# Optimization experiments

Hardware: AMD Instinct MI355X
Metric: run time of the kernel (lower is better)

## Reference

```python
import jax, jax.numpy as jnp
import numpy as np

B, T, N, H, D = 8, 128, 170, 4, 16
F = H * D  # 64
LN_EPS = 1e-5
MASK_FILL = -(2.0 ** 15) + 1.0  # -32767, matches torch code


def setup_inputs() -> dict:
    key = jax.random.key(0)
    ks = jax.random.split(key, 16)
    s = 0.05
    def w(k):
        return jax.random.normal(k, (F, F), jnp.float32) * s
    def b(k):
        return jax.random.normal(k, (F,), jnp.float32) * s
    return {
        "x": jax.random.normal(ks[0], (B, T, N, F), jnp.float32),
        "te": jax.random.normal(ks[1], (B, T, N, F), jnp.float32),
        "Wq": w(ks[2]), "bq": b(ks[3]),
        "Wk": w(ks[4]), "bk": b(ks[5]),
        "Wv": w(ks[6]), "bv": b(ks[7]),
        "Wo": w(ks[8]), "bo": b(ks[9]),
        "Wf1": w(ks[10]), "bf1": b(ks[11]),
        "Wf2": w(ks[12]), "bf2": b(ks[13]),
    }


def _ln(v):
    # LayerNorm over last dim, elementwise_affine=False
    m = jnp.mean(v, axis=-1, keepdims=True)
    var = jnp.mean((v - m) ** 2, axis=-1, keepdims=True)
    return (v - m) / jnp.sqrt(var + LN_EPS)


def reference(x, te, Wq, bq, Wk, bk, Wv, bv, Wo, bo, Wf1, bf1, Wf2, bf2):
    x = x + te  # [B,T,N,F]
    # q/k/v projections (FeedForward with L=1 -> plain linear, no ReLU)
    q = (x @ Wq + bq).reshape(B, T, N, H, D)
    k = (x @ Wk + bk).reshape(B, T, N, H, D)
    v = (x @ Wv + bv).reshape(B, T, N, H, D)
    # attention over time axis, independent per node n and head h
    att = jnp.einsum('btnhd,bsnhd->bhnts', q, k) / jnp.sqrt(jnp.float32(D))
    causal = jnp.tril(jnp.ones((T, T), dtype=bool))  # keep s <= t
    att = jnp.where(causal[None, None, None, :, :], att, MASK_FILL)
    att = jax.nn.softmax(att, axis=-1)
    out = jnp.einsum('bhnts,bsnhd->btnhd', att, v).reshape(B, T, N, F)
    out = out @ Wo + bo  # ofc
    val = _ln(out + x)
    # ff: Linear-ReLU-Linear with residual + LN (res_ln=True)
    ff = jax.nn.relu(val @ Wf1 + bf1) @ Wf2 + bf2
    return _ln(ff + val)
```

## Files before the change

### kernel.cpp

```cpp
#include <hip/hip_runtime.h>

typedef __attribute__((ext_vector_type(8))) short short8;
typedef __attribute__((ext_vector_type(4))) float f32x4;
typedef __attribute__((ext_vector_type(16))) float f32x16;

#define B_ 8
#define T_ 128
#define N_ 170
#define F_ 64
#define ROWSTRIDE (N_ * F_)

union U4 { unsigned u[4]; short8 s; };

__device__ __forceinline__ unsigned short f2bf(float f) {
    union { float f; unsigned u; } v; v.f = f;
    unsigned r = v.u + 0x7fffu + ((v.u >> 16) & 1u);
    return (unsigned short)(r >> 16);
}
__device__ __forceinline__ unsigned cvtpk(float lo, float hi) {
    unsigned d;
    asm("v_cvt_pk_bf16_f32 %0, %1, %2" : "=v"(d) : "v"(lo), "v"(hi));
    return d;
}
__device__ __forceinline__ int swz128(int row, int byteInRow) {
    return row * 128 + (byteInRow ^ ((row & 7) << 4));
}
__device__ __forceinline__ int swz256(int row, int byteInRow) {
    return row * 256 + (byteInRow ^ ((row & 15) << 4));
}
__device__ __forceinline__ short8 ldfrag16(const char* base, int row0, int kbyte, int lane) {
    int row = row0 + (lane & 15);
    return *(const short8*)(base + swz128(row, kbyte + ((lane >> 4) << 4)));
}
__device__ __forceinline__ short8 ldfrag16w(const char* base, int row0, int kbyte, int lane) {
    int row = row0 + (lane & 15);
    return *(const short8*)(base + swz256(row, kbyte + ((lane >> 4) << 4)));
}
__device__ __forceinline__ short8 ldfrag32(const char* base, int row0, int colbyte, int lane) {
    int row = row0 + (lane & 31);
    return *(const short8*)(base + swz128(row, colbyte + ((lane >> 5) << 4)));
}
__device__ __forceinline__ short8 wfragT(const unsigned short* __restrict__ wT, int nt, int kc, int lane) {
    int j  = nt * 16 + (lane & 15);
    int k0 = kc * 32 + ((lane >> 4) & 3) * 8;
    return *(const short8*)(wT + j * 64 + k0);
}
__device__ __forceinline__ f32x4 zero4() {
    f32x4 v = {0.f, 0.f, 0.f, 0.f};
    return v;
}
__device__ __forceinline__ f32x16 zero16() {
    f32x16 v = {0.f, 0.f, 0.f, 0.f, 0.f, 0.f, 0.f, 0.f,
                0.f, 0.f, 0.f, 0.f, 0.f, 0.f, 0.f, 0.f};
    return v;
}
__device__ __forceinline__ float rmax16(const f32x16& v) {
    float a0 = fmaxf(v[0], v[1]),  a1 = fmaxf(v[2], v[3]);
    float a2 = fmaxf(v[4], v[5]),  a3 = fmaxf(v[6], v[7]);
    float a4 = fmaxf(v[8], v[9]),  a5 = fmaxf(v[10], v[11]);
    float a6 = fmaxf(v[12], v[13]), a7 = fmaxf(v[14], v[15]);
    float b0 = fmaxf(a0, a1), b1 = fmaxf(a2, a3);
    float b2 = fmaxf(a4, a5), b3 = fmaxf(a6, a7);
    return fmaxf(fmaxf(b0, b1), fmaxf(b2, b3));
}
__device__ __forceinline__ float rsum16(const f32x16& v) {
    float a0 = v[0] + v[1],  a1 = v[2] + v[3];
    float a2 = v[4] + v[5],  a3 = v[6] + v[7];
    float a4 = v[8] + v[9],  a5 = v[10] + v[11];
    float a6 = v[12] + v[13], a7 = v[14] + v[15];
    float b0 = a0 + a1, b1 = a2 + a3, b2 = a4 + a5, b3 = a6 + a7;
    return (b0 + b1) + (b2 + b3);
}

__device__ __forceinline__ void lnS(float (&z)[2][4][4]) {
#pragma unroll
    for (int mi = 0; mi < 2; ++mi) {
        float s = 0.f;
#pragma unroll
        for (int nt = 0; nt < 4; ++nt)
#pragma unroll
        for (int r = 0; r < 4; ++r) s += z[mi][nt][r];
        s += __shfl_xor(s, 16); s += __shfl_xor(s, 32);
        float mean = s * 0.015625f;
        float q = 0.f;
#pragma unroll
        for (int nt = 0; nt < 4; ++nt)
#pragma unroll
        for (int r = 0; r < 4; ++r) { z[mi][nt][r] -= mean; q += z[mi][nt][r] * z[mi][nt][r]; }
        q += __shfl_xor(q, 16); q += __shfl_xor(q, 32);
        float rstd = __builtin_amdgcn_rsqf(q * 0.015625f + 1e-5f);
#pragma unroll
        for (int nt = 0; nt < 4; ++nt)
#pragma unroll
        for (int r = 0; r < 4; ++r) z[mi][nt][r] *= rstd;
    }
}

__global__ void prep_weights(const float* __restrict__ Wq, const float* __restrict__ Wk,
                             const float* __restrict__ Wv, const float* __restrict__ Wo,
                             const float* __restrict__ Wf1, const float* __restrict__ Wf2,
                             unsigned short* __restrict__ ws) {
    const float* Ws[6] = {Wq, Wk, Wv, Wo, Wf1, Wf2};
    const float* W = Ws[blockIdx.x];
    unsigned short* o = ws + blockIdx.x * 4096;
#pragma unroll
    for (int i = 0; i < 16; ++i) {
        int idx = i * 256 + threadIdx.x;
        int j = idx >> 6, k = idx & 63;
        o[idx] = f2bf(W[k * 64 + j]);
    }
}

__global__ __launch_bounds__(256, 3)
void ta_fused(const float* __restrict__ x, const float* __restrict__ te,
              const unsigned short* __restrict__ wT,
              const float* __restrict__ bq, const float* __restrict__ bk,
              const float* __restrict__ bv, const float* __restrict__ bo,
              const float* __restrict__ bf1, const float* __restrict__ bf2,
              float* __restrict__ out)
{
    __shared__ __align__(16) char sKb[16384];
    __shared__ __align__(16) char sVt[16384];
    __shared__ __align__(16) char sBn[16384];

    const int tid  = threadIdx.x;
    const int lane = tid & 63;
    const int wv   = tid >> 6;
    const int lam  = lane & 15;
    const int g    = (lane >> 4) & 3;
    const int bid  = blockIdx.x;
    const int b    = bid / N_;
    const int n    = bid - b * N_;
    const long long base = ((long long)b * T_ * N_ + n) * F_;
    const int t0w = wv * 32;
    char* myb = sBn + wv * 4096;

    short8 ax[2][2];
#pragma unroll
    for (int mi = 0; mi < 2; ++mi) {
        const float* xr = x  + base + (long long)(t0w + mi * 16 + lam) * ROWSTRIDE;
        const float* tr = te + base + (long long)(t0w + mi * 16 + lam) * ROWSTRIDE;
#pragma unroll
        for (int kc = 0; kc < 2; ++kc) {
            int f0 = kc * 32 + g * 8;
            float4 a0 = *(const float4*)(xr + f0);
            float4 a1 = *(const float4*)(xr + f0 + 4);
            float4 c0 = *(const float4*)(tr + f0);
            float4 c1 = *(const float4*)(tr + f0 + 4);
            U4 u;
            u.u[0] = cvtpk(a0.x + c0.x, a0.y + c0.y);
            u.u[1] = cvtpk(a0.z + c0.z, a0.w + c0.w);
            u.u[2] = cvtpk(a1.x + c1.x, a1.y + c1.y);
            u.u[3] = cvtpk(a1.z + c1.z, a1.w + c1.w);
            ax[mi][kc] = u.s;
        }
    }

    {
#pragma unroll
        for (int w = 0; w < 3; ++w) {
            const unsigned short* wTp = wT + w * 4096;
            short8 bw[4][2];
#pragma unroll
            for (int nt = 0; nt < 4; ++nt) {
                bw[nt][0] = wfragT(wTp, nt, 0, lane);
                bw[nt][1] = wfragT(wTp, nt, 1, lane);
            }
            f32x4 acc[2][4];
#pragma unroll
            for (int mi = 0; mi < 2; ++mi)
#pragma unroll
            for (int nt = 0; nt < 4; ++nt) acc[mi][nt] = zero4();

            if (w < 2) {
                const float* bp = (w == 0) ? bq : bk;
                float4 bj[4];
#pragma unroll
                for (int nt = 0; nt < 4; ++nt) bj[nt] = *(const float4*)(bp + nt * 16 + g * 4);
#pragma unroll
                for (int kc = 0; kc < 2; ++kc)
#pragma unroll
                for (int mi = 0; mi < 2; ++mi)
#pragma unroll
                for (int nt = 0; nt < 4; ++nt)
                    acc[mi][nt] = __builtin_amdgcn_mfma_f32_16x16x32_bf16(bw[nt][kc], ax[mi][kc], acc[mi][nt], 0, 0, 0);
#pragma unroll
                for (int mi = 0; mi < 2; ++mi)
#pragma unroll
                for (int nt = 0; nt < 4; ++nt) {
                    unsigned d0 = cvtpk(acc[mi][nt][0] + bj[nt].x, acc[mi][nt][1] + bj[nt].y);
                    unsigned d1 = cvtpk(acc[mi][nt][2] + bj[nt].z, acc[mi][nt][3] + bj[nt].w);
                    unsigned long long pk = (unsigned long long)d0 | ((unsigned long long)d1 << 32);
                    if (w == 0) {
                        *(unsigned long long*)(myb + swz128(mi * 16 + lam, (nt * 16 + g * 4) * 2)) = pk;
                    } else {
                        *(unsigned long long*)(sKb + swz128(t0w + mi * 16 + lam, (nt * 16 + g * 4) * 2)) = pk;
                    }
                }
            } else {
                float bias[4];
#pragma unroll
                for (int nt = 0; nt < 4; ++nt) bias[nt] = bv[nt * 16 + lam];
#pragma unroll
                for (int kc = 0; kc < 2; ++kc)
#pragma unroll
                for (int mi = 0; mi < 2; ++mi)
#pragma unroll
                for (int nt = 0; nt < 4; ++nt)
                    acc[mi][nt] = __builtin_amdgcn_mfma_f32_16x16x32_bf16(ax[mi][kc], bw[nt][kc], acc[mi][nt], 0, 0, 0);
#pragma unroll
                for (int mi = 0; mi < 2; ++mi)
#pragma unroll
                for (int nt = 0; nt < 4; ++nt) {
                    int f   = nt * 16 + lam;
                    int tb0 = t0w + mi * 16 + g * 4;
                    unsigned d0 = cvtpk(acc[mi][nt][0] + bias[nt], acc[mi][nt][1] + bias[nt]);
                    unsigned d1 = cvtpk(acc[mi][nt][2] + bias[nt], acc[mi][nt][3] + bias[nt]);
                    unsigned long long pkv = (unsigned long long)d0 | ((unsigned long long)d1 << 32);
                    *(unsigned long long*)(sVt + swz256(f, tb0 * 2)) = pkv;
                }
            }
        }
    }
    __syncthreads();

    float4 rxv[2][4], rtv[2][4];
#pragma unroll
    for (int mi = 0; mi < 2; ++mi)
#pragma unroll
    for (int nt = 0; nt < 4; ++nt) {
        long long roff = base + (long long)(t0w + mi * 16 + lam) * ROWSTRIDE + nt * 16 + g * 4;
        rxv[mi][nt] = *(const float4*)(x + roff);
        rtv[mi][nt] = *(const float4*)(te + roff);
    }

    {
        const int tcol = lane & 31;
        const int hi4  = (lane >> 5) * 4;
        f32x4 oaccT[4][2];
#pragma unroll
        for (int h = 0; h < 4; ++h) { oaccT[h][0] = zero4(); oaccT[h][1] = zero4(); }

#pragma unroll
        for (int h = 0; h < 4; ++h) {
            short8 qf = ldfrag32(myb, 0, h * 32, lane);
            f32x16 sacc[4];
            __builtin_amdgcn_s_setprio(1);
#pragma unroll
            for (int sb = 0; sb < 4; ++sb) {
                if (sb > wv) continue;
                short8 kf = ldfrag32(sKb, sb * 32, h * 32, lane);
                sacc[sb] = __builtin_amdgcn_mfma_f32_32x32x16_bf16(kf, qf, zero16(), 0, 0, 0);
            }
            __builtin_amdgcn_s_setprio(0);
#pragma unroll
            for (int sb = 0; sb < 4; ++sb) {
                if (sb != wv) continue;
#pragma unroll
                for (int r = 0; r < 16; ++r) {
                    int srow = (r & 3) + 8 * (r >> 2) + hi4;
                    if (srow > tcol) sacc[sb][r] = -3.0e38f;
                }
            }
            float m = -3.0e38f;
#pragma unroll
            for (int sb = 0; sb < 4; ++sb) {
                if (sb > wv) continue;
                m = fmaxf(m, rmax16(sacc[sb]));
            }
            m = fmaxf(m, __shfl_xor(m, 32));
            float sum = 0.f;
#pragma unroll
            for (int sb = 0; sb < 4; ++sb) {
                if (sb > wv) continue;
#pragma unroll
                for (int r = 0; r < 16; ++r)
                    sacc[sb][r] = __expf((sacc[sb][r] - m) * 0.25f);
                sum += rsum16(sacc[sb]);
            }
            sum += __shfl_xor(sum, 32);
            float rs = __builtin_amdgcn_rcpf(sum);

#pragma unroll
            for (int sb = 0; sb < 4; ++sb) {
                if (sb > wv) continue;
                float ps[16];
#pragma unroll
                for (int r = 0; r < 16; ++r) ps[r] = sacc[sb][r] * rs;
                unsigned a0 = cvtpk(ps[0],  ps[1]);
                unsigned a1 = cvtpk(ps[4],  ps[5]);
                unsigned a2 = cvtpk(ps[8],  ps[9]);
                unsigned a3 = cvtpk(ps[12], ps[13]);
                unsigned b0 = cvtpk(ps[2],  ps[3]);
                unsigned b1 = cvtpk(ps[6],  ps[7]);
                unsigned b2 = cvtpk(ps[10], ps[11]);
                unsigned b3 = cvtpk(ps[14], ps[15]);
                asm("v_permlane32_swap_b32 %0, %1" : "+v"(a0), "+v"(a2));
                asm("v_permlane32_swap_b32 %0, %1" : "+v"(a1), "+v"(a3));
                asm("v_permlane16_swap_b32 %0, %1" : "+v"(a0), "+v"(a1));
                asm("v_permlane16_swap_b32 %0, %1" : "+v"(a2), "+v"(a3));
                asm("v_permlane32_swap_b32 %0, %1" : "+v"(b0), "+v"(b2));
                asm("v_permlane32_swap_b32 %0, %1" : "+v"(b1), "+v"(b3));
                asm("v_permlane16_swap_b32 %0, %1" : "+v"(b0), "+v"(b1));
                asm("v_permlane16_swap_b32 %0, %1" : "+v"(b2), "+v"(b3));
                U4 F0, F1;
                F0.u[0] = a0; F0.u[1] = b0; F0.u[2] = a2; F0.u[3] = b2;
                F1.u[0] = a1; F1.u[1] = b1; F1.u[2] = a3; F1.u[3] = b3;
                short8 vf = ldfrag16w(sVt, h * 16, sb * 64, lane);
                __builtin_amdgcn_s_setprio(1);
                oaccT[h][0] = __builtin_amdgcn_mfma_f32_16x16x32_bf16(vf, F0.s, oaccT[h][0], 0, 0, 0);
                oaccT[h][1] = __builtin_amdgcn_mfma_f32_16x16x32_bf16(vf, F1.s, oaccT[h][1], 0, 0, 0);
                __builtin_amdgcn_s_setprio(0);
            }
        }

#pragma unroll
        for (int h = 0; h < 4; ++h)
#pragma unroll
        for (int mi = 0; mi < 2; ++mi) {
            unsigned d0 = cvtpk(oaccT[h][mi][0], oaccT[h][mi][1]);
            unsigned d1 = cvtpk(oaccT[h][mi][2], oaccT[h][mi][3]);
            unsigned long long pk = (unsigned long long)d0 | ((unsigned long long)d1 << 32);
            *(unsigned long long*)(myb + swz128(mi * 16 + lam, (h * 16 + g * 4) * 2)) = pk;
        }
    }

    float val[2][4][4];
    {
        short8 af[2][2];
#pragma unroll
        for (int mi = 0; mi < 2; ++mi)
#pragma unroll
        for (int kc = 0; kc < 2; ++kc) af[mi][kc] = ldfrag16(myb, mi * 16, kc * 64, lane);
        const unsigned short* wTp = wT + 3 * 4096;
        short8 bwf[4][2]; float4 bj[4];
#pragma unroll
        for (int nt = 0; nt < 4; ++nt) {
            bwf[nt][0] = wfragT(wTp, nt, 0, lane);
            bwf[nt][1] = wfragT(wTp, nt, 1, lane);
            bj[nt]     = *(const float4*)(bo + nt * 16 + g * 4);
        }
        f32x4 acc[2][4];
#pragma unroll
        for (int mi = 0; mi < 2; ++mi)
#pragma unroll
        for (int nt = 0; nt < 4; ++nt) acc[mi][nt] = zero4();
#pragma unroll
        for (int kc = 0; kc < 2; ++kc)
#pragma unroll
        for (int mi = 0; mi < 2; ++mi)
#pragma unroll
        for (int nt = 0; nt < 4; ++nt)
            acc[mi][nt] = __builtin_amdgcn_mfma_f32_16x16x32_bf16(bwf[nt][kc], af[mi][kc], acc[mi][nt], 0, 0, 0);
#pragma unroll
        for (int mi = 0; mi < 2; ++mi)
#pragma unroll
        for (int nt = 0; nt < 4; ++nt) {
            val[mi][nt][0] = acc[mi][nt][0] + bj[nt].x + rxv[mi][nt].x + rtv[mi][nt].x;
            val[mi][nt][1] = acc[mi][nt][1] + bj[nt].y + rxv[mi][nt].y + rtv[mi][nt].y;
            val[mi][nt][2] = acc[mi][nt][2] + bj[nt].z + rxv[mi][nt].z + rtv[mi][nt].z;
            val[mi][nt][3] = acc[mi][nt][3] + bj[nt].w + rxv[mi][nt].w + rtv[mi][nt].w;
        }
        lnS(val);
#pragma unroll
        for (int mi = 0; mi < 2; ++mi)
#pragma unroll
        for (int nt = 0; nt < 4; ++nt) {
            unsigned d0 = cvtpk(val[mi][nt][0], val[mi][nt][1]);
            unsigned d1 = cvtpk(val[mi][nt][2], val[mi][nt][3]);
            unsigned long long pk = (unsigned long long)d0 | ((unsigned long long)d1 << 32);
            *(unsigned long long*)(myb + swz128(mi * 16 + lam, (nt * 16 + g * 4) * 2)) = pk;
        }
    }

    {
        short8 af[2][2];
#pragma unroll
        for (int mi = 0; mi < 2; ++mi)
#pragma unroll
        for (int kc = 0; kc < 2; ++kc) af[mi][kc] = ldfrag16(myb, mi * 16, kc * 64, lane);
        const unsigned short* wTp = wT + 4 * 4096;
        short8 bwf[4][2]; float4 bj[4];
#pragma unroll
        for (int nt = 0; nt < 4; ++nt) {
            bwf[nt][0] = wfragT(wTp, nt, 0, lane);
            bwf[nt][1] = wfragT(wTp, nt, 1, lane);
            bj[nt]     = *(const float4*)(bf1 + nt * 16 + g * 4);
        }
        f32x4 acc[2][4];
#pragma unroll
        for (int mi = 0; mi < 2; ++mi)
#pragma unroll
        for (int nt = 0; nt < 4; ++nt) acc[mi][nt] = zero4();
#pragma unroll
        for (int kc = 0; kc < 2; ++kc)
#pragma unroll
        for (int mi = 0; mi < 2; ++mi)
#pragma unroll
        for (int nt = 0; nt < 4; ++nt)
            acc[mi][nt] = __builtin_amdgcn_mfma_f32_16x16x32_bf16(bwf[nt][kc], af[mi][kc], acc[mi][nt], 0, 0, 0);
#pragma unroll
        for (int mi = 0; mi < 2; ++mi)
#pragma unroll
        for (int nt = 0; nt < 4; ++nt) {
            unsigned d0 = cvtpk(fmaxf(acc[mi][nt][0] + bj[nt].x, 0.f), fmaxf(acc[mi][nt][1] + bj[nt].y, 0.f));
            unsigned d1 = cvtpk(fmaxf(acc[mi][nt][2] + bj[nt].z, 0.f), fmaxf(acc[mi][nt][3] + bj[nt].w, 0.f));
            unsigned long long pk = (unsigned long long)d0 | ((unsigned long long)d1 << 32);
            *(unsigned long long*)(myb + swz128(mi * 16 + lam, (nt * 16 + g * 4) * 2)) = pk;
        }
    }

    {
        short8 af[2][2];
#pragma unroll
        for (int mi = 0; mi < 2; ++mi)
#pragma unroll
        for (int kc = 0; kc < 2; ++kc) af[mi][kc] = ldfrag16(myb, mi * 16, kc * 64, lane);
        const unsigned short* wTp = wT + 5 * 4096;
        short8 bwf[4][2]; float4 bj[4];
#pragma unroll
        for (int nt = 0; nt < 4; ++nt) {
            bwf[nt][0] = wfragT(wTp, nt, 0, lane);
            bwf[nt][1] = wfragT(wTp, nt, 1, lane);
            bj[nt]     = *(const float4*)(bf2 + nt * 16 + g * 4);
        }
        f32x4 acc[2][4];
#pragma unroll
        for (int mi = 0; mi < 2; ++mi)
#pragma unroll
        for (int nt = 0; nt < 4; ++nt) acc[mi][nt] = zero4();
#pragma unroll
        for (int kc = 0; kc < 2; ++kc)
#pragma unroll
        for (int mi = 0; mi < 2; ++mi)
#pragma unroll
        for (int nt = 0; nt < 4; ++nt)
            acc[mi][nt] = __builtin_amdgcn_mfma_f32_16x16x32_bf16(bwf[nt][kc], af[mi][kc], acc[mi][nt], 0, 0, 0);
        float z[2][4][4];
#pragma unroll
        for (int mi = 0; mi < 2; ++mi)
#pragma unroll
        for (int nt = 0; nt < 4; ++nt) {
            z[mi][nt][0] = acc[mi][nt][0] + bj[nt].x + val[mi][nt][0];
            z[mi][nt][1] = acc[mi][nt][1] + bj[nt].y + val[mi][nt][1];
            z[mi][nt][2] = acc[mi][nt][2] + bj[nt].z + val[mi][nt][2];
            z[mi][nt][3] = acc[mi][nt][3] + bj[nt].w + val[mi][nt][3];
        }
        lnS(z);
#pragma unroll
        for (int mi = 0; mi < 2; ++mi)
#pragma unroll
        for (int nt = 0; nt < 4; ++nt) {
            float4 o = {z[mi][nt][0], z[mi][nt][1], z[mi][nt][2], z[mi][nt][3]};
            *(float4*)(out + base + (long long)(t0w + mi * 16 + lam) * ROWSTRIDE + nt * 16 + g * 4) = o;
        }
    }
}

extern "C" void kernel_launch(void* const* d_in, const int* in_sizes, int n_in,
                              void* d_out, int out_size, void* d_ws, size_t ws_size,
                              hipStream_t stream) {
    const float* x   = (const float*)d_in[0];
    const float* te  = (const float*)d_in[1];
    const float* Wq  = (const float*)d_in[2];
    const float* bq  = (const float*)d_in[3];
    const float* Wk  = (const float*)d_in[4];
    const float* bk  = (const float*)d_in[5];
    const float* Wv  = (const float*)d_in[6];
    const float* bv  = (const float*)d_in[7];
    const float* Wo  = (const float*)d_in[8];
    const float* bo  = (const float*)d_in[9];
    const float* Wf1 = (const float*)d_in[10];
    const float* bf1 = (const float*)d_in[11];
    const float* Wf2 = (const float*)d_in[12];
    const float* bf2 = (const float*)d_in[13];
    unsigned short* wsT = (unsigned short*)d_ws;

    prep_weights<<<dim3(6), dim3(256), 0, stream>>>(Wq, Wk, Wv, Wo, Wf1, Wf2, wsT);
    ta_fused<<<dim3(B_ * N_), dim3(256), 0, stream>>>(
        x, te, wsT, bq, bk, bv, bo, bf1, bf2, (float*)d_out);
}
```

Before: 89.33 us.

## Drop per-wave scratch LDS buffer, reuse K buffer and raise occupancy to 4

Removes the 16KB per-block scratch shared buffer. Q is staged through the K buffer and loaded into registers before K overwrites it, and later stages (attention output, LN output, FFN hidden) reuse the K region after an added barrier. The residual x/te reload moves from before attention to the output projection epilogue. Launch bounds rise to 4 blocks per CU to get more waves resident in the smaller LDS footprint. The cost is an extra __syncthreads, re-reading x/te later, holding Q fragments in registers, and a tighter register budget that may cause spills.

```diff
diff --git a/kernel.cpp b/kernel.cpp
--- a/kernel.cpp
+++ b/kernel.cpp
@@ -111,7 +111,7 @@
     }
 }
 
-__global__ __launch_bounds__(256, 3)
+__global__ __launch_bounds__(256, 4)
 void ta_fused(const float* __restrict__ x, const float* __restrict__ te,
               const unsigned short* __restrict__ wT,
               const float* __restrict__ bq, const float* __restrict__ bk,
@@ -121,7 +121,6 @@
 {
     __shared__ __align__(16) char sKb[16384];
     __shared__ __align__(16) char sVt[16384];
-    __shared__ __align__(16) char sBn[16384];
 
     const int tid  = threadIdx.x;
     const int lane = tid & 63;
@@ -133,7 +132,6 @@
     const int n    = bid - b * N_;
     const long long base = ((long long)b * T_ * N_ + n) * F_;
     const int t0w = wv * 32;
-    char* myb = sBn + wv * 4096;
 
     short8 ax[2][2];
 #pragma unroll
@@ -156,101 +154,125 @@
         }
     }
 
+    short8 qf[4];
+
     {
-#pragma unroll
-        for (int w = 0; w < 3; ++w) {
-            const unsigned short* wTp = wT + w * 4096;
-            short8 bw[4][2];
+        {
+            const unsigned short* wTp = wT;
+            short8 bw[4][2]; float4 bj[4];
 #pragma unroll
             for (int nt = 0; nt < 4; ++nt) {
                 bw[nt][0] = wfragT(wTp, nt, 0, lane);
                 bw[nt][1] = wfragT(wTp, nt, 1, lane);
+                bj[nt]    = *(const float4*)(bq + nt * 16 + g * 4);
             }
             f32x4 acc[2][4];
 #pragma unroll
             for (int mi = 0; mi < 2; ++mi)
 #pragma unroll
             for (int nt = 0; nt < 4; ++nt) acc[mi][nt] = zero4();
-
-            if (w < 2) {
-                const float* bp = (w == 0) ? bq : bk;
-                float4 bj[4];
-#pragma unroll
-                for (int nt = 0; nt < 4; ++nt) bj[nt] = *(const float4*)(bp + nt * 16 + g * 4);
-#pragma unroll
-                for (int kc = 0; kc < 2; ++kc)
-#pragma unroll
-                for (int mi = 0; mi < 2; ++mi)
-#pragma unroll
-                for (int nt = 0; nt < 4; ++nt)
-                    acc[mi][nt] = __builtin_amdgcn_mfma_f32_16x16x32_bf16(bw[nt][kc], ax[mi][kc], acc[mi][nt], 0, 0, 0);
-#pragma unroll
-                for (int mi = 0; mi < 2; ++mi)
-#pragma unroll
-                for (int nt = 0; nt < 4; ++nt) {
-                    unsigned d0 = cvtpk(acc[mi][nt][0] + bj[nt].x, acc[mi][nt][1] + bj[nt].y);
-                    unsigned d1 = cvtpk(acc[mi][nt][2] + bj[nt].z, acc[mi][nt][3] + bj[nt].w);
-                    unsigned long long pk = (unsigned long long)d0 | ((unsigned long long)d1 << 32);
-                    if (w == 0) {
-                        *(unsigned long long*)(myb + swz128(mi * 16 + lam, (nt * 16 + g * 4) * 2)) = pk;
-                    } else {
-                        *(unsigned long long*)(sKb + swz128(t0w + mi * 16 + lam, (nt * 16 + g * 4) * 2)) = pk;
-                    }
-                }
-            } else {
-                float bias[4];
-#pragma unroll
-                for (int nt = 0; nt < 4; ++nt) bias[nt] = bv[nt * 16 + lam];
-#pragma unroll
-                for (int kc = 0; kc < 2; ++kc)
-#pragma unroll
-                for (int mi = 0; mi < 2; ++mi)
-#pragma unroll
-                for (int nt = 0; nt < 4; ++nt)
-                    acc[mi][nt] = __builtin_amdgcn_mfma_f32_16x16x32_bf16(ax[mi][kc], bw[nt][kc], acc[mi][nt], 0, 0, 0);
-#pragma unroll
-                for (int mi = 0; mi < 2; ++mi)
-#pragma unroll
-                for (int nt = 0; nt < 4; ++nt) {
-                    int f   = nt * 16 + lam;
-                    int tb0 = t0w + mi * 16 + g * 4;
-                    unsigned d0 = cvtpk(acc[mi][nt][0] + bias[nt], acc[mi][nt][1] + bias[nt]);
-                    unsigned d1 = cvtpk(acc[mi][nt][2] + bias[nt], acc[mi][nt][3] + bias[nt]);
-                    unsigned long long pkv = (unsigned long long)d0 | ((unsigned long long)d1 << 32);
-                    *(unsigned long long*)(sVt + swz256(f, tb0 * 2)) = pkv;
-                }
+#pragma unroll
+            for (int kc = 0; kc < 2; ++kc)
+#pragma unroll
+            for (int mi = 0; mi < 2; ++mi)
+#pragma unroll
+            for (int nt = 0; nt < 4; ++nt)
+                acc[mi][nt] = __builtin_amdgcn_mfma_f32_16x16x32_bf16(bw[nt][kc], ax[mi][kc], acc[mi][nt], 0, 0, 0);
+#pragma unroll
+            for (int mi = 0; mi < 2; ++mi)
+#pragma unroll
+            for (int nt = 0; nt < 4; ++nt) {
+                unsigned d0 = cvtpk(acc[mi][nt][0] + bj[nt].x, acc[mi][nt][1] + bj[nt].y);
+                unsigned d1 = cvtpk(acc[mi][nt][2] + bj[nt].z, acc[mi][nt][3] + bj[nt].w);
+                unsigned long long pk = (unsigned long long)d0 | ((unsigned long long)d1 << 32);
+                *(unsigned long long*)(sKb + swz128(t0w + mi * 16 + lam, (nt * 16 + g * 4) * 2)) = pk;
+            }
+#pragma unroll
+            for (int h = 0; h < 4; ++h) qf[h] = ldfrag32(sKb, t0w, h * 32, lane);
+        }
+        {
+            const unsigned short* wTp = wT + 4096;
+            short8 bw[4][2]; float4 bj[4];
+#pragma unroll
+            for (int nt = 0; nt < 4; ++nt) {
+                bw[nt][0] = wfragT(wTp, nt, 0, lane);
+                bw[nt][1] = wfragT(wTp, nt, 1, lane);
+                bj[nt]    = *(const float4*)(bk + nt * 16 + g * 4);
+            }
+            f32x4 acc[2][4];
+#pragma unroll
+            for (int mi = 0; mi < 2; ++mi)
+#pragma unroll
+            for (int nt = 0; nt < 4; ++nt) acc[mi][nt] = zero4();
+#pragma unroll
+            for (int kc = 0; kc < 2; ++kc)
+#pragma unroll
+            for (int mi = 0; mi < 2; ++mi)
+#pragma unroll
+            for (int nt = 0; nt < 4; ++nt)
+                acc[mi][nt] = __builtin_amdgcn_mfma_f32_16x16x32_bf16(bw[nt][kc], ax[mi][kc], acc[mi][nt], 0, 0, 0);
+#pragma unroll
+            for (int mi = 0; mi < 2; ++mi)
+#pragma unroll
+            for (int nt = 0; nt < 4; ++nt) {
+                unsigned d0 = cvtpk(acc[mi][nt][0] + bj[nt].x, acc[mi][nt][1] + bj[nt].y);
+                unsigned d1 = cvtpk(acc[mi][nt][2] + bj[nt].z, acc[mi][nt][3] + bj[nt].w);
+                unsigned long long pk = (unsigned long long)d0 | ((unsigned long long)d1 << 32);
+                *(unsigned long long*)(sKb + swz128(t0w + mi * 16 + lam, (nt * 16 + g * 4) * 2)) = pk;
+            }
+        }
+        {
+            const unsigned short* wTp = wT + 2 * 4096;
+            short8 bw[4][2]; float bias[4];
+#pragma unroll
+            for (int nt = 0; nt < 4; ++nt) {
+                bw[nt][0] = wfragT(wTp, nt, 0, lane);
+                bw[nt][1] = wfragT(wTp, nt, 1, lane);
+                bias[nt]  = bv[nt * 16 + lam];
+            }
+            f32x4 acc[2][4];
+#pragma unroll
+            for (int mi = 0; mi < 2; ++mi)
+#pragma unroll
+            for (int nt = 0; nt < 4; ++nt) acc[mi][nt] = zero4();
+#pragma unroll
+            for (int kc = 0; kc < 2; ++kc)
+#pragma unroll
+            for (int mi = 0; mi < 2; ++mi)
+#pragma unroll
+            for (int nt = 0; nt < 4; ++nt)
+                acc[mi][nt] = __builtin_amdgcn_mfma_f32_16x16x32_bf16(ax[mi][kc], bw[nt][kc], acc[mi][nt], 0, 0, 0);
+#pragma unroll
+            for (int mi = 0; mi < 2; ++mi)
+#pragma unroll
+            for (int nt = 0; nt < 4; ++nt) {
+                int f   = nt * 16 + lam;
+                int tb0 = t0w + mi * 16 + g * 4;
+                unsigned d0 = cvtpk(acc[mi][nt][0] + bias[nt], acc[mi][nt][1] + bias[nt]);
+                unsigned d1 = cvtpk(acc[mi][nt][2] + bias[nt], acc[mi][nt][3] + bias[nt]);
+                unsigned long long pkv = (unsigned long long)d0 | ((unsigned long long)d1 << 32);
+                *(unsigned long long*)(sVt + swz256(f, tb0 * 2)) = pkv;
             }
         }
     }
     __syncthreads();
 
-    float4 rxv[2][4], rtv[2][4];
-#pragma unroll
-    for (int mi = 0; mi < 2; ++mi)
-#pragma unroll
-    for (int nt = 0; nt < 4; ++nt) {
-        long long roff = base + (long long)(t0w + mi * 16 + lam) * ROWSTRIDE + nt * 16 + g * 4;
-        rxv[mi][nt] = *(const float4*)(x + roff);
-        rtv[mi][nt] = *(const float4*)(te + roff);
-    }
-
+    f32x4 oaccT[4][2];
     {
         const int tcol = lane & 31;
         const int hi4  = (lane >> 5) * 4;
-        f32x4 oaccT[4][2];
 #pragma unroll
         for (int h = 0; h < 4; ++h) { oaccT[h][0] = zero4(); oaccT[h][1] = zero4(); }
 
 #pragma unroll
         for (int h = 0; h < 4; ++h) {
-            short8 qf = ldfrag32(myb, 0, h * 32, lane);
             f32x16 sacc[4];
             __builtin_amdgcn_s_setprio(1);
 #pragma unroll
             for (int sb = 0; sb < 4; ++sb) {
                 if (sb > wv) continue;
                 short8 kf = ldfrag32(sKb, sb * 32, h * 32, lane);
-                sacc[sb] = __builtin_amdgcn_mfma_f32_32x32x16_bf16(kf, qf, zero16(), 0, 0, 0);
+                sacc[sb] = __builtin_amdgcn_mfma_f32_32x32x16_bf16(kf, qf[h], zero16(), 0, 0, 0);
             }
             __builtin_amdgcn_s_setprio(0);
 #pragma unroll
@@ -313,16 +335,17 @@
                 __builtin_amdgcn_s_setprio(0);
             }
         }
-
-#pragma unroll
-        for (int h = 0; h < 4; ++h)
-#pragma unroll
-        for (int mi = 0; mi < 2; ++mi) {
-            unsigned d0 = cvtpk(oaccT[h][mi][0], oaccT[h][mi][1]);
-            unsigned d1 = cvtpk(oaccT[h][mi][2], oaccT[h][mi][3]);
-            unsigned long long pk = (unsigned long long)d0 | ((unsigned long long)d1 << 32);
-            *(unsigned long long*)(myb + swz128(mi * 16 + lam, (h * 16 + g * 4) * 2)) = pk;
-        }
+    }
+    __syncthreads();
+
+#pragma unroll
+    for (int h = 0; h < 4; ++h)
+#pragma unroll
+    for (int mi = 0; mi < 2; ++mi) {
+        unsigned d0 = cvtpk(oaccT[h][mi][0], oaccT[h][mi][1]);
+        unsigned d1 = cvtpk(oaccT[h][mi][2], oaccT[h][mi][3]);
+        unsigned long long pk = (unsigned long long)d0 | ((unsigned long long)d1 << 32);
+        *(unsigned long long*)(sKb + swz128(t0w + mi * 16 + lam, (h * 16 + g * 4) * 2)) = pk;
     }
 
     float val[2][4][4];
@@ -331,7 +354,7 @@
 #pragma unroll
         for (int mi = 0; mi < 2; ++mi)
 #pragma unroll
-        for (int kc = 0; kc < 2; ++kc) af[mi][kc] = ldfrag16(myb, mi * 16, kc * 64, lane);
+        for (int kc = 0; kc < 2; ++kc) af[mi][kc] = ldfrag16(sKb, t0w + mi * 16, kc * 64, lane);
         const unsigned short* wTp = wT + 3 * 4096;
         short8 bwf[4][2]; float4 bj[4];
 #pragma unroll
@@ -356,10 +379,13 @@
         for (int mi = 0; mi < 2; ++mi)
 #pragma unroll
         for (int nt = 0; nt < 4; ++nt) {
-            val[mi][nt][0] = acc[mi][nt][0] + bj[nt].x + rxv[mi][nt].x + rtv[mi][nt].x;
-            val[mi][nt][1] = acc[mi][nt][1] + bj[nt].y + rxv[mi][nt].y + rtv[mi][nt].y;
-            val[mi][nt][2] = acc[mi][nt][2] + bj[nt].z + rxv[mi][nt].z + rtv[mi][nt].z;
-            val[mi][nt][3] = acc[mi][nt][3] + bj[nt].w + rxv[mi][nt].w + rtv[mi][nt].w;
+            long long roff = base + (long long)(t0w + mi * 16 + lam) * ROWSTRIDE + nt * 16 + g * 4;
+            float4 xv = *(const float4*)(x + roff);
+            float4 tv = *(const float4*)(te + roff);
+            val[mi][nt][0] = acc[mi][nt][0] + bj[nt].x + xv.x + tv.x;
+            val[mi][nt][1] = acc[mi][nt][1] + bj[nt].y + xv.y + tv.y;
+            val[mi][nt][2] = acc[mi][nt][2] + bj[nt].z + xv.z + tv.z;
+            val[mi][nt][3] = acc[mi][nt][3] + bj[nt].w + xv.w + tv.w;
         }
         lnS(val);
 #pragma unroll
@@ -369,7 +395,7 @@
             unsigned d0 = cvtpk(val[mi][nt][0], val[mi][nt][1]);
             unsigned d1 = cvtpk(val[mi][nt][2], val[mi][nt][3]);
             unsigned long long pk = (unsigned long long)d0 | ((unsigned long long)d1 << 32);
-            *(unsigned long long*)(myb + swz128(mi * 16 + lam, (nt * 16 + g * 4) * 2)) = pk;
+            *(unsigned long long*)(sKb + swz128(t0w + mi * 16 + lam, (nt * 16 + g * 4) * 2)) = pk;
         }
     }
 
@@ -378,7 +404,7 @@
 #pragma unroll
         for (int mi = 0; mi < 2; ++mi)
 #pragma unroll
-        for (int kc = 0; kc < 2; ++kc) af[mi][kc] = ldfrag16(myb, mi * 16, kc * 64, lane);
+        for (int kc = 0; kc < 2; ++kc) af[mi][kc] = ldfrag16(sKb, t0w + mi * 16, kc * 64, lane);
         const unsigned short* wTp = wT + 4 * 4096;
         short8 bwf[4][2]; float4 bj[4];
 #pragma unroll
@@ -406,7 +432,7 @@
             unsigned d0 = cvtpk(fmaxf(acc[mi][nt][0] + bj[nt].x, 0.f), fmaxf(acc[mi][nt][1] + bj[nt].y, 0.f));
             unsigned d1 = cvtpk(fmaxf(acc[mi][nt][2] + bj[nt].z, 0.f), fmaxf(acc[mi][nt][3] + bj[nt].w, 0.f));
             unsigned long long pk = (unsigned long long)d0 | ((unsigned long long)d1 << 32);
-            *(unsigned long long*)(myb + swz128(mi * 16 + lam, (nt * 16 + g * 4) * 2)) = pk;
+            *(unsigned long long*)(sKb + swz128(t0w + mi * 16 + lam, (nt * 16 + g * 4) * 2)) = pk;
         }
     }
 
@@ -415,7 +441,7 @@
 #pragma unroll
         for (int mi = 0; mi < 2; ++mi)
 #pragma unroll
-        for (int kc = 0; kc < 2; ++kc) af[mi][kc] = ldfrag16(myb, mi * 16, kc * 64, lane);
+        for (int kc = 0; kc < 2; ++kc) af[mi][kc] = ldfrag16(sKb, t0w + mi * 16, kc * 64, lane);
         const unsigned short* wTp = wT + 5 * 4096;
         short8 bwf[4][2]; float4 bj[4];
 #pragma unroll
```

Result: no change. 88.32 us (-1.1%).
